# Kernel tuning notes

Hardware: AMD Instinct MI355X
Metric: run time of the kernel (lower is better)

The kernel has to match this reference:

```python
import jax, jax.numpy as jnp
import numpy as np
from functools import partial

L, H, D, T_MAX = 12, 12, 768, 256
HD = D // H
FULL = 302  # 100+100+30+72
LN_EPS = 1e-5


def _ln(x, g, b):
    m = jnp.mean(x, axis=-1, keepdims=True)
    v = jnp.mean((x - m) ** 2, axis=-1, keepdims=True)
    return (x - m) * jax.lax.rsqrt(v + LN_EPS) * g + b


def setup_inputs() -> dict:
    key = jax.random.key(0)
    ks = iter(jax.random.split(key, 40))
    B, T = 64, 256
    w = lambda *s: jax.random.normal(next(ks), s, dtype=jnp.float32) * 0.02
    inp = {
        'idxs': jax.random.randint(next(ks), (B, T, 4), 0, 30, dtype=jnp.int32),
        'lat_emb': w(100, 192), 'lon_emb': w(100, 192),
        'sog_emb': w(30, 192), 'cog_emb': w(72, 192),
        'pos_emb': jnp.zeros((1, T_MAX, D), jnp.float32),
        'ln1_g': jnp.ones((L, D)), 'ln1_b': jnp.zeros((L, D)),
        'ln2_g': jnp.ones((L, D)), 'ln2_b': jnp.zeros((L, D)),
        'Wq': w(L, D, D), 'bq': jnp.zeros((L, D)),
        'Wk': w(L, D, D), 'bk': jnp.zeros((L, D)),
        'Wv': w(L, D, D), 'bv': jnp.zeros((L, D)),
        'Wo': w(L, D, D), 'bo': jnp.zeros((L, D)),
        'W1': w(L, D, 4 * D), 'b1': jnp.zeros((L, 4 * D)),
        'W2': w(L, 4 * D, D), 'b2': jnp.zeros((L, D)),
        'lnf_g': jnp.ones((D,)), 'lnf_b': jnp.zeros((D,)),
        'Whead': w(D, FULL),
    }
    return inp


def _transformer(idxs, lat_emb, lon_emb, sog_emb, cog_emb, pos_emb,
                 ln1_g, ln1_b, ln2_g, ln2_b, Wq, bq, Wk, bk, Wv, bv, Wo, bo,
                 W1, b1, W2, b2, lnf_g, lnf_b, Whead):
    B, T, _ = idxs.shape
    # four-hot embedding: concat of the four attribute embeddings -> [B,T,768]
    h = jnp.concatenate([
        lat_emb[idxs[..., 0]], lon_emb[idxs[..., 1]],
        sog_emb[idxs[..., 2]], cog_emb[idxs[..., 3]],
    ], axis=-1) + pos_emb[:, :T]
    causal = jnp.tril(jnp.ones((T, T), dtype=bool))  # [T,T]
    scale = 1.0 / np.sqrt(HD)

    def block(h, p):
        (g1, b1_, g2, b2_, wq, bq_, wk, bk_, wv, bv_, wo, bo_,
         w1, bf1, w2, bf2) = p
        x = _ln(h, g1, b1_)
        q = (x @ wq + bq_).reshape(B, T, H, HD)
        k = (x @ wk + bk_).reshape(B, T, H, HD)
        v = (x @ wv + bv_).reshape(B, T, H, HD)
        att = jnp.einsum('bqhd,bkhd->bhqk', q, k) * scale
        att = jnp.where(causal, att, -jnp.inf)
        att = jax.nn.softmax(att, axis=-1)
        y = jnp.einsum('bhqk,bkhd->bqhd', att, v).reshape(B, T, D)
        h = h + y @ wo + bo_
        x = _ln(h, g2, b2_)
        h = h + jax.nn.gelu(x @ w1 + bf1, approximate=False) @ w2 + bf2
        return h, None

    stacked = (ln1_g, ln1_b, ln2_g, ln2_b, Wq, bq, Wk, bk, Wv, bv, Wo, bo,
               W1, b1, W2, b2)
    h, _ = jax.lax.scan(block, h, stacked)
    h = _ln(h, lnf_g, lnf_b)
    return h @ Whead  # [B,T,302] logits


def reference(idxs, lat_emb, lon_emb, sog_emb, cog_emb, pos_emb,
              ln1_g, ln1_b, ln2_g, ln2_b, Wq, bq, Wk, bk, Wv, bv, Wo, bo,
              W1, b1, W2, b2, lnf_g, lnf_b, Whead):
    return _transformer(idxs, lat_emb, lon_emb, sog_emb, cog_emb, pos_emb,
                        ln1_g, ln1_b, ln2_g, ln2_b, Wq, bq, Wk, bk, Wv, bv,
                        Wo, bo, W1, b1, W2, b2, lnf_g, lnf_b, Whead)
```

## Files before the change

### kernel.cpp

```cpp
#include <hip/hip_runtime.h>
#include <math.h>


#define LNUM 12
#define HNUM 12
#define DDIM 768
#define HDIM 64
#define TSEQ 256
#define NTOK 16384
#define DFF  3072
#define QKS  1536
#define NOUTC 302
#define NOUTP 384

typedef unsigned short u16;
typedef __attribute__((ext_vector_type(8))) __bf16 bf16x8;
typedef __attribute__((ext_vector_type(8))) unsigned short u16x8;
typedef __attribute__((ext_vector_type(4))) float f32x4;

__device__ __forceinline__ u16 f2bf(float f) {
    union { float f; unsigned u; } v; v.f = f;
    return (u16)((v.u + 0x7fff + ((v.u >> 16) & 1)) >> 16);
}

__device__ __forceinline__ void gl2lds16(const u16* g, u16* l) {
    __builtin_amdgcn_global_load_lds(
        (const __attribute__((address_space(1))) void*)g,
        (__attribute__((address_space(3))) void*)l, 16, 0, 0);
}

__global__ __launch_bounds__(256)
void embed_kernel(const int* __restrict__ idxs, const float* __restrict__ lat,
                  const float* __restrict__ lon, const float* __restrict__ sog,
                  const float* __restrict__ cog, const float* __restrict__ pos,
                  float* __restrict__ h) {
    int i = blockIdx.x * 256 + threadIdx.x;
    int tok = i / DDIM, d = i - tok * DDIM;
    int t = tok & (TSEQ - 1);
    int tab = d / 192, sub = d - tab * 192;
    const float* tp = (tab == 0) ? lat : (tab == 1) ? lon : (tab == 2) ? sog : cog;
    int row = idxs[tok * 4 + tab];
    h[i] = tp[row * 192 + sub] + pos[t * DDIM + d];
}

__global__ __launch_bounds__(256)
void ln_kernel(const float* __restrict__ in, u16* __restrict__ out,
               const float* __restrict__ g, const float* __restrict__ b) {
    const int row = blockIdx.x, t = threadIdx.x;
    const float* x = in + (size_t)row * DDIM;
    float v0 = x[t], v1 = x[t + 256], v2 = x[t + 512];
    float s = v0 + v1 + v2;
    float sq = v0 * v0 + v1 * v1 + v2 * v2;
    #pragma unroll
    for (int m = 32; m; m >>= 1) { s += __shfl_xor(s, m); sq += __shfl_xor(sq, m); }
    __shared__ float red[8];
    const int w = t >> 6;
    if ((t & 63) == 0) { red[w] = s; red[4 + w] = sq; }
    __syncthreads();
    s  = red[0] + red[1] + red[2] + red[3];
    sq = red[4] + red[5] + red[6] + red[7];
    const float mean = s * (1.f / DDIM);
    const float rstd = rsqrtf(sq * (1.f / DDIM) - mean * mean + 1e-5f);
    u16* o = out + (size_t)row * DDIM;
    o[t]       = f2bf((v0 - mean) * rstd * g[t]       + b[t]);
    o[t + 256] = f2bf((v1 - mean) * rstd * g[t + 256] + b[t + 256]);
    o[t + 512] = f2bf((v2 - mean) * rstd * g[t + 512] + b[t + 512]);
}

__global__ __launch_bounds__(256)
void wconv_kernel(const float* __restrict__ in, u16* __restrict__ out,
                  int R, int C, int Cpad) {
    __shared__ float tile[32][33];
    const float* src = in + (size_t)blockIdx.z * R * C;
    u16* dst = out + (size_t)blockIdx.z * (size_t)Cpad * R;
    const int c0 = blockIdx.x * 32, r0 = blockIdx.y * 32;
    const int tx = threadIdx.x & 31, ty = threadIdx.x >> 5;
    #pragma unroll
    for (int i = 0; i < 4; ++i) {
        int r = r0 + ty + i * 8, c = c0 + tx;
        tile[ty + i * 8][tx] = (c < C) ? src[(size_t)r * C + c] : 0.f;
    }
    __syncthreads();
    #pragma unroll
    for (int i = 0; i < 4; ++i) {
        int oc = c0 + ty + i * 8;
        dst[(size_t)oc * R + r0 + tx] = f2bf(tile[tx][ty + i * 8]);
    }
}

template <int MODE>
__global__ __launch_bounds__(256)
void gemm_bt(const u16* __restrict__ A, const u16* __restrict__ Bt,
             const float* __restrict__ bias, const float* __restrict__ bias2,
             const float* __restrict__ bias3, const float* __restrict__ res,
             void* __restrict__ Cout, int M, int N, int K, int ncut) {
    __shared__ u16 As[3][128][32] __attribute__((aligned(16)));
    __shared__ u16 Bs[3][128][32] __attribute__((aligned(16)));
    const int t = threadIdx.x;
    const int w = t >> 6, lane = t & 63;
    const int bm = blockIdx.x * 128, bn = blockIdx.y * 128;
    const int moff = (w >> 1) * 64, noff = (w & 1) * 64;
    const int lrow = t >> 2, lcol = (t & 3) * 8;
    const int fm = lane & 15, fq = lane >> 4;
    const f32x4 zero = {0.f, 0.f, 0.f, 0.f};
    f32x4 acc[4][4];
    #pragma unroll
    for (int a = 0; a < 4; ++a)
        #pragma unroll
        for (int c = 0; c < 4; ++c) acc[a][c] = zero;
    const u16* pA = A + (size_t)(bm + lrow) * K + lcol;
    const u16* pB = Bt + (size_t)(bn + lrow) * K + lcol;
    const size_t rstep = (size_t)64 * K;
    const int wr = w << 4;
    auto stage = [&](int s, int b) {
        const u16* ga = pA + s * 32;
        const u16* gb = pB + s * 32;
        gl2lds16(ga,         &As[b][wr][0]);
        gl2lds16(ga + rstep, &As[b][wr + 64][0]);
        gl2lds16(gb,         &Bs[b][wr][0]);
        gl2lds16(gb + rstep, &Bs[b][wr + 64][0]);
    };
    const int kts = K >> 5;
    stage(0, 0);
    stage(1, 1);
    int bcur = 0, bpre = 2;
    for (int kt = 0; kt < kts; ++kt) {
        if (kt + 2 < kts) stage(kt + 2, bpre);
        const int ahead = kts - 1 - kt;
        if (ahead >= 2)      asm volatile("s_waitcnt vmcnt(8)" ::: "memory");
        else if (ahead == 1) asm volatile("s_waitcnt vmcnt(4)" ::: "memory");
        else                 asm volatile("s_waitcnt vmcnt(0)" ::: "memory");
        __builtin_amdgcn_s_barrier();
        bf16x8 af[4], bfr[4];
        #pragma unroll
        for (int mt = 0; mt < 4; ++mt)
            af[mt] = __builtin_bit_cast(bf16x8, *(const u16x8*)&As[bcur][moff + mt * 16 + fm][fq * 8]);
        #pragma unroll
        for (int nt = 0; nt < 4; ++nt)
            bfr[nt] = __builtin_bit_cast(bf16x8, *(const u16x8*)&Bs[bcur][noff + nt * 16 + fm][fq * 8]);
        asm volatile("s_waitcnt lgkmcnt(0)" ::: "memory");
        __builtin_amdgcn_s_barrier();
        #pragma unroll
        for (int mt = 0; mt < 4; ++mt)
            #pragma unroll
            for (int nt = 0; nt < 4; ++nt)
                acc[mt][nt] = __builtin_amdgcn_mfma_f32_16x16x32_bf16(af[mt], bfr[nt], acc[mt][nt], 0, 0, 0);
        bcur = (bcur == 2) ? 0 : bcur + 1;
        bpre = (bpre == 2) ? 0 : bpre + 1;
    }
    #pragma unroll
    for (int mt = 0; mt < 4; ++mt) {
        #pragma unroll
        for (int nt = 0; nt < 4; ++nt) {
            const int col = bn + noff + nt * 16 + fm;
            float bv = 0.f;
            if (MODE == 5) {
                bv = (col < 768) ? bias[col] : (col < 1536) ? bias2[col - 768] : bias3[col - 1536];
            } else if (MODE != 3) {
                bv = bias[col];
            }
            #pragma unroll
            for (int i = 0; i < 4; ++i) {
                const int row = bm + moff + mt * 16 + fq * 4 + i;
                float v = acc[mt][nt][i] + bv;
                if (MODE == 0) {
                    ((u16*)Cout)[(size_t)row * N + col] = f2bf(v);
                } else if (MODE == 1) {
                    v = 0.5f * v * (1.f + erff(v * 0.70710678118654752f));
                    ((u16*)Cout)[(size_t)row * N + col] = f2bf(v);
                } else if (MODE == 2) {
                    ((float*)Cout)[(size_t)row * N + col] = v + res[(size_t)row * N + col];
                } else if (MODE == 3) {
                    if (col < ncut) ((float*)Cout)[(size_t)row * ncut + col] = v;
                } else {
                    if (col < 1536) {
                        ((u16*)Cout)[(size_t)row * QKS + col] = f2bf(v);
                    } else {
                        const int c = col - 1536;
                        const int bb = row >> 8, tt = row & 255;
                        const int hh = c >> 6, dd = c & 63;
                        u16* vt = (u16*)Cout + (size_t)NTOK * QKS;
                        vt[(((size_t)(bb * HNUM + hh)) * HDIM + dd) * TSEQ + tt] = f2bf(v);
                    }
                }
            }
        }
    }
}

__global__ __launch_bounds__(256)
void attn_kernel(const u16* __restrict__ QK, const u16* __restrict__ Vt,
                 u16* __restrict__ Yb) {
    __shared__ u16 Pt[4][256][16] __attribute__((aligned(16)));
    const int bh = blockIdx.x;
    const int b = bh / HNUM, hh = bh - b * HNUM;
    const int w = threadIdx.x >> 6, lane = threadIdx.x & 63;
    const int fm = lane & 15, fq = lane >> 4;
    const int qt = blockIdx.y * 4 + w;
    const size_t qrow0 = (size_t)b * TSEQ;
    const int col0 = hh * HDIM;
    const u16* qp = QK + (qrow0 + qt * 16 + fm) * QKS + col0 + fq * 8;
    const bf16x8 aq0 = __builtin_bit_cast(bf16x8, *(const u16x8*)qp);
    const bf16x8 aq1 = __builtin_bit_cast(bf16x8, *(const u16x8*)(qp + 32));
    f32x4 s[16];
    #pragma unroll
    for (int kt = 0; kt < 16; ++kt) {
        if (kt <= qt) {
            const u16* kp = QK + (qrow0 + kt * 16 + fm) * QKS + 768 + col0 + fq * 8;
            bf16x8 bk0 = __builtin_bit_cast(bf16x8, *(const u16x8*)kp);
            bf16x8 bk1 = __builtin_bit_cast(bf16x8, *(const u16x8*)(kp + 32));
            f32x4 z = {0.f, 0.f, 0.f, 0.f};
            z = __builtin_amdgcn_mfma_f32_16x16x32_bf16(aq0, bk0, z, 0, 0, 0);
            z = __builtin_amdgcn_mfma_f32_16x16x32_bf16(aq1, bk1, z, 0, 0, 0);
            s[kt] = z;
        }
    }
    float lrow[4];
    #pragma unroll
    for (int i = 0; i < 4; ++i) {
        float mx = -1e30f;
        #pragma unroll
        for (int kt = 0; kt < 16; ++kt) {
            if (kt <= qt) {
                const bool valid = (kt < qt) || (fm <= fq * 4 + i);
                const float v = valid ? s[kt][i] * 0.125f : -1e30f;
                s[kt][i] = v;
                mx = fmaxf(mx, v);
            }
        }
        #pragma unroll
        for (int d = 1; d < 16; d <<= 1) mx = fmaxf(mx, __shfl_xor(mx, d));
        float sum = 0.f;
        #pragma unroll
        for (int kt = 0; kt < 16; ++kt) {
            if (kt <= qt) {
                const float e = __expf(s[kt][i] - mx);
                s[kt][i] = e;
                sum += e;
            }
        }
        #pragma unroll
        for (int d = 1; d < 16; d <<= 1) sum += __shfl_xor(sum, d);
        lrow[i] = sum;
    }
    const int nks = (qt + 2) >> 1;
    #pragma unroll
    for (int kt = 0; kt < 16; ++kt) {
        if (kt < 2 * nks) {
            unsigned lo = 0, hi = 0;
            if (kt <= qt) {
                lo = (unsigned)f2bf(s[kt][0]) | ((unsigned)f2bf(s[kt][1]) << 16);
                hi = (unsigned)f2bf(s[kt][2]) | ((unsigned)f2bf(s[kt][3]) << 16);
            }
            uint2 pk; pk.x = lo; pk.y = hi;
            *(uint2*)&Pt[w][kt * 16 + fm][fq * 4] = pk;
        }
    }
    __syncthreads();
    f32x4 o[4];
    #pragma unroll
    for (int dt = 0; dt < 4; ++dt) o[dt] = (f32x4){0.f, 0.f, 0.f, 0.f};
    #pragma unroll
    for (int ks = 0; ks < 8; ++ks) {
        if (ks < nks) {
            u16x8 praw;
            #pragma unroll
            for (int j = 0; j < 8; ++j) praw[j] = Pt[w][ks * 32 + fq * 8 + j][fm];
            const bf16x8 pa = __builtin_bit_cast(bf16x8, praw);
            #pragma unroll
            for (int dt = 0; dt < 4; ++dt) {
                const u16* vp = Vt + ((size_t)bh * HDIM + dt * 16 + fm) * TSEQ + ks * 32 + fq * 8;
                const bf16x8 bv = __builtin_bit_cast(bf16x8, *(const u16x8*)vp);
                o[dt] = __builtin_amdgcn_mfma_f32_16x16x32_bf16(pa, bv, o[dt], 0, 0, 0);
            }
        }
    }
    #pragma unroll
    for (int i = 0; i < 4; ++i) {
        const float inv = 1.f / lrow[i];
        #pragma unroll
        for (int dt = 0; dt < 4; ++dt)
            Yb[(qrow0 + qt * 16 + fq * 4 + i) * DDIM + col0 + dt * 16 + fm] = f2bf(o[dt][i] * inv);
    }
}

extern "C" void kernel_launch(void* const* d_in, const int* in_sizes, int n_in,
                              void* d_out, int out_size, void* d_ws, size_t ws_size,
                              hipStream_t stream) {
    (void)in_sizes; (void)n_in; (void)out_size; (void)ws_size;
    const int*   idxs  = (const int*)d_in[0];
    const float* lat   = (const float*)d_in[1];
    const float* lon   = (const float*)d_in[2];
    const float* sog   = (const float*)d_in[3];
    const float* cog   = (const float*)d_in[4];
    const float* pos   = (const float*)d_in[5];
    const float* ln1_g = (const float*)d_in[6];
    const float* ln1_b = (const float*)d_in[7];
    const float* ln2_g = (const float*)d_in[8];
    const float* ln2_b = (const float*)d_in[9];
    const float* Wq = (const float*)d_in[10];
    const float* bq = (const float*)d_in[11];
    const float* Wk = (const float*)d_in[12];
    const float* bk = (const float*)d_in[13];
    const float* Wv = (const float*)d_in[14];
    const float* bv = (const float*)d_in[15];
    const float* Wo = (const float*)d_in[16];
    const float* bo = (const float*)d_in[17];
    const float* W1 = (const float*)d_in[18];
    const float* b1 = (const float*)d_in[19];
    const float* W2 = (const float*)d_in[20];
    const float* b2 = (const float*)d_in[21];
    const float* lnf_g = (const float*)d_in[22];
    const float* lnf_b = (const float*)d_in[23];
    const float* Whead = (const float*)d_in[24];

    char* base = (char*)d_ws;
    size_t off = 0;
    auto carve = [&](size_t bytes) { void* r = base + off; off += (bytes + 255) & ~(size_t)255; return r; };
    float* h  = (float*)carve((size_t)NTOK * DDIM * 4);
    u16* xb = (u16*)carve((size_t)NTOK * DDIM * 2);
    u16* qk = (u16*)carve((size_t)NTOK * QKS * 2);
    u16* vt = (u16*)carve((size_t)NTOK * DDIM * 2);
    u16* yb = (u16*)carve((size_t)NTOK * DDIM * 2);
    u16* ub = qk;
    u16* WtQKV = (u16*)carve((size_t)3 * DDIM * DDIM * 2);
    u16* WtO = (u16*)carve((size_t)DDIM * DDIM * 2);
    u16* Wt1 = (u16*)carve((size_t)DDIM * DFF * 2);
    u16* Wt2 = (u16*)carve((size_t)DFF * DDIM * 2);
    u16* WtH = (u16*)carve((size_t)NOUTP * DDIM * 2);

    embed_kernel<<<NTOK * DDIM / 256, 256, 0, stream>>>(idxs, lat, lon, sog, cog, pos, h);

    const dim3 g768(128, 6), g3072(128, 24), gqkv(128, 18), ghead(128, 3);
    const dim3 tq(24, 24, 1), t1(96, 24, 1), t2(24, 96, 1);
    const size_t wsq = (size_t)DDIM * DDIM, wsf = (size_t)DDIM * DFF;
    for (int l = 0; l < LNUM; ++l) {
        wconv_kernel<<<tq, 256, 0, stream>>>(Wq + l * wsq, WtQKV, DDIM, DDIM, DDIM);
        wconv_kernel<<<tq, 256, 0, stream>>>(Wk + l * wsq, WtQKV + wsq, DDIM, DDIM, DDIM);
        wconv_kernel<<<tq, 256, 0, stream>>>(Wv + l * wsq, WtQKV + 2 * wsq, DDIM, DDIM, DDIM);
        wconv_kernel<<<tq, 256, 0, stream>>>(Wo + l * wsq, WtO, DDIM, DDIM, DDIM);
        wconv_kernel<<<t1, 256, 0, stream>>>(W1 + l * wsf, Wt1, DDIM, DFF, DFF);
        wconv_kernel<<<t2, 256, 0, stream>>>(W2 + l * wsf, Wt2, DFF, DDIM, DDIM);

        ln_kernel<<<NTOK, 256, 0, stream>>>(h, xb, ln1_g + l * DDIM, ln1_b + l * DDIM);
        gemm_bt<5><<<gqkv, 256, 0, stream>>>(xb, WtQKV, bq + l * DDIM, bk + l * DDIM,
                                             bv + l * DDIM, nullptr, qk,
                                             NTOK, 3 * DDIM, DDIM, 0);
        attn_kernel<<<dim3(768, 4), 256, 0, stream>>>(qk, vt, yb);
        gemm_bt<2><<<g768, 256, 0, stream>>>(yb, WtO, bo + l * DDIM, nullptr, nullptr, h, h,
                                             NTOK, DDIM, DDIM, 0);
        ln_kernel<<<NTOK, 256, 0, stream>>>(h, xb, ln2_g + l * DDIM, ln2_b + l * DDIM);
        gemm_bt<1><<<g3072, 256, 0, stream>>>(xb, Wt1, b1 + l * DFF, nullptr, nullptr, nullptr, ub,
                                              NTOK, DFF, DDIM, 0);
        gemm_bt<2><<<g768, 256, 0, stream>>>(ub, Wt2, b2 + l * DDIM, nullptr, nullptr, h, h,
                                             NTOK, DDIM, DFF, 0);
    }
    ln_kernel<<<NTOK, 256, 0, stream>>>(h, xb, lnf_g, lnf_b);
    wconv_kernel<<<dim3(NOUTP / 32, DDIM / 32, 1), 256, 0, stream>>>(Whead, WtH, DDIM, NOUTC, NOUTP);
    gemm_bt<3><<<ghead, 256, 0, stream>>>(xb, WtH, nullptr, nullptr, nullptr, nullptr, d_out,
                                          NTOK, NOUTP, DDIM, NOUTC);
}
```

Measured before the change: 6.656 ms.

## Replace 128x128 GEMMs with 256x256-tile 8-wave kernel using direct global-to-LDS loads

Adds a gemm256 kernel with 256x256 output tiles, 512 threads (8 waves), K-step 64, and double-buffered LDS filled through direct global-to-LDS copies with an XOR-swizzled layout. It interleaves MFMA quadrants with staged loads, uses explicit vmcnt waits, s_setprio, and an XCD-aware block remap. The aim is more data reuse per tile and better overlap of loads with compute for the QKV, output-projection and MLP GEMMs. The cost is heavy register use (128 accumulator floats per thread), only 64x3 blocks for the 768-wide GEMMs, and reliance on the gl2lds16 helper and hand-tuned barriers being correct.

```diff
diff --git a/kernel.cpp b/kernel.cpp
--- a/kernel.cpp
+++ b/kernel.cpp
@@ -85,6 +85,135 @@
     for (int i = 0; i < 4; ++i) {
         int oc = c0 + ty + i * 8;
         dst[(size_t)oc * R + r0 + tx] = f2bf(tile[tx][ty + i * 8]);
+    }
+}
+
+
+#define LDA8(MQ) \
+  _Pragma("unroll") for (int mt = 0; mt < 4; ++mt) { \
+    a[mt][0] = __builtin_bit_cast(bf16x8, *(const u16x8*)(A0p + (MQ)*8192 + mt*1024)); \
+    a[mt][1] = __builtin_bit_cast(bf16x8, *(const u16x8*)(A1p + (MQ)*8192 + mt*1024)); }
+
+#define LDB4(NQ, BR) \
+  _Pragma("unroll") for (int nt = 0; nt < 2; ++nt) { \
+    BR[nt][0] = __builtin_bit_cast(bf16x8, *(const u16x8*)(B0p + (NQ)*8192 + nt*1024)); \
+    BR[nt][1] = __builtin_bit_cast(bf16x8, *(const u16x8*)(B1p + (NQ)*8192 + nt*1024)); }
+
+#define MMA16(MQ, NQ, BR) \
+  __builtin_amdgcn_s_barrier(); \
+  asm volatile("s_waitcnt lgkmcnt(0)" ::: "memory"); \
+  __builtin_amdgcn_s_setprio(1); \
+  _Pragma("unroll") for (int mt = 0; mt < 4; ++mt) \
+  _Pragma("unroll") for (int nt = 0; nt < 2; ++nt) { \
+    acc[(MQ)*4+mt][(NQ)*2+nt] = __builtin_amdgcn_mfma_f32_16x16x32_bf16(a[mt][0], BR[nt][0], acc[(MQ)*4+mt][(NQ)*2+nt], 0, 0, 0); \
+    acc[(MQ)*4+mt][(NQ)*2+nt] = __builtin_amdgcn_mfma_f32_16x16x32_bf16(a[mt][1], BR[nt][1], acc[(MQ)*4+mt][(NQ)*2+nt], 0, 0, 0); } \
+  __builtin_amdgcn_s_setprio(0);
+
+#define STGA(NXT, H, KT) { \
+  const u16* s_ = gA + (size_t)((H) * 128) * K + (size_t)(KT) * 64; \
+  u16* d_ = &Sh[NXT][H][0][0] + w * 512; \
+  gl2lds16(s_, d_); gl2lds16(s_ + (size_t)64 * K, d_ + 4096); }
+
+#define STGB(NXT, H, KT) { \
+  const u16* s_ = gB + (size_t)((H) * 128) * K + (size_t)(KT) * 64; \
+  u16* d_ = &Sh[NXT][2 + (H)][0][0] + w * 512; \
+  gl2lds16(s_, d_); gl2lds16(s_ + (size_t)64 * K, d_ + 4096); }
+
+#define VM4 asm volatile("s_waitcnt vmcnt(4)" ::: "memory");
+#define VM2 asm volatile("s_waitcnt vmcnt(2)" ::: "memory");
+#define VM0 asm volatile("s_waitcnt vmcnt(0)" ::: "memory");
+#define VMN
+
+#define KTILE(CUR, KT, STG, VA, VB, VC) { \
+  const u16* A0p = aQ0 + (CUR) * 32768; const u16* A1p = aQ1 + (CUR) * 32768; \
+  const u16* B0p = bQ0 + (CUR) * 32768; const u16* B1p = bQ1 + (CUR) * 32768; \
+   LDA8(0) LDB4(0, b0) if (STG) STGA(1 - (CUR), 0, (KT) + 1) \
+         MMA16(0, 0, b0) VA __builtin_amdgcn_s_barrier(); \
+   LDB4(1, b1) if (STG) STGB(1 - (CUR), 0, (KT) + 1) \
+         MMA16(0, 1, b1) VB __builtin_amdgcn_s_barrier(); \
+   LDA8(1) if (STG) STGB(1 - (CUR), 1, (KT) + 1) \
+         MMA16(1, 1, b1) __builtin_amdgcn_s_barrier(); \
+   if (STG) STGA(1 - (CUR), 1, (KT) + 1) \
+         MMA16(1, 0, b0) VC __builtin_amdgcn_s_barrier(); \
+}
+
+template <int MODE>
+__global__ __launch_bounds__(512, 2)
+void gemm256(const u16* __restrict__ A, const u16* __restrict__ Bt,
+             const float* __restrict__ bias, const float* __restrict__ bias2,
+             const float* __restrict__ bias3, const float* __restrict__ res,
+             void* __restrict__ Cout, int M, int N, int K) {
+    (void)M;
+    __shared__ u16 Sh[2][4][128][64] __attribute__((aligned(16)));
+    const int t = threadIdx.x;
+    const int w = t >> 6, l = t & 63;
+    const int wm = w >> 2, wn = w & 3;
+    const int fm = l & 15, fq = l >> 4;
+    const int nwg = (int)(gridDim.x * gridDim.y);
+    int lin = (int)(blockIdx.y * gridDim.x + blockIdx.x);
+    const int cpx = nwg >> 3;
+    lin = (lin & 7) * cpx + (lin >> 3);
+    const int bm = (lin & 63) * 256, bn = (lin >> 6) * 256;
+    const int srow = (w << 3) + (l >> 3);
+    const int schunk = (l & 7) ^ ((l >> 3) & 7);
+    const u16* gA = A + (size_t)(bm + srow) * K + schunk * 8;
+    const u16* gB = Bt + (size_t)(bn + srow) * K + schunk * 8;
+    const int aoff0 = fm * 64 + ((fq ^ (fm & 7)) << 3);
+    const int aoff1 = aoff0 ^ 32;
+    const u16* aQ0 = &Sh[0][0][0][0] + wm * 4096 + aoff0;
+    const u16* aQ1 = &Sh[0][0][0][0] + wm * 4096 + aoff1;
+    const u16* bQ0 = &Sh[0][2][0][0] + wn * 2048 + aoff0;
+    const u16* bQ1 = &Sh[0][2][0][0] + wn * 2048 + aoff1;
+    f32x4 acc[8][4];
+    #pragma unroll
+    for (int i = 0; i < 8; ++i)
+        #pragma unroll
+        for (int j = 0; j < 4; ++j) acc[i][j] = (f32x4){0.f, 0.f, 0.f, 0.f};
+    bf16x8 a[4][2], b0[2][2], b1[2][2];
+    STGA(0, 0, 0) STGB(0, 0, 0) STGB(0, 1, 0) STGA(0, 1, 0)
+    asm volatile("s_waitcnt vmcnt(4)" ::: "memory");
+    __builtin_amdgcn_s_barrier();
+    const int nkt = K >> 6;
+    for (int kt = 0; kt < nkt - 2; kt += 2) {
+        KTILE(0, kt,     true, VM4, VM4, VM4)
+        KTILE(1, kt + 1, true, VM4, VM4, VM4)
+    }
+    KTILE(0, nkt - 2, true,  VM4, VM4, VM4)
+    KTILE(1, nkt - 1, false, VM2, VM0, VMN)
+    #pragma unroll
+    for (int m8 = 0; m8 < 8; ++m8) {
+        const int row0 = bm + (m8 >> 2) * 128 + wm * 64 + (m8 & 3) * 16 + fq * 4;
+        #pragma unroll
+        for (int n4 = 0; n4 < 4; ++n4) {
+            const int col = bn + (n4 >> 1) * 128 + wn * 32 + (n4 & 1) * 16 + fm;
+            float bv;
+            if (MODE == 5) {
+                bv = (col < 768) ? bias[col] : (col < 1536) ? bias2[col - 768] : bias3[col - 1536];
+            } else {
+                bv = bias[col];
+            }
+            #pragma unroll
+            for (int i = 0; i < 4; ++i) {
+                const int row = row0 + i;
+                float v = acc[m8][n4][i] + bv;
+                if (MODE == 1) {
+                    v = 0.5f * v * (1.f + erff(v * 0.70710678118654752f));
+                    ((u16*)Cout)[(size_t)row * N + col] = f2bf(v);
+                } else if (MODE == 2) {
+                    ((float*)Cout)[(size_t)row * N + col] = v + res[(size_t)row * N + col];
+                } else {
+                    if (col < 1536) {
+                        ((u16*)Cout)[(size_t)row * QKS + col] = f2bf(v);
+                    } else {
+                        const int c = col - 1536;
+                        const int bb = row >> 8, tt = row & 255;
+                        const int hh = c >> 6, dd = c & 63;
+                        u16* vt = (u16*)Cout + (size_t)NTOK * QKS;
+                        vt[(((size_t)(bb * HNUM + hh)) * HDIM + dd) * TSEQ + tt] = f2bf(v);
+                    }
+                }
+            }
+        }
     }
 }
 
@@ -331,7 +460,7 @@
 
     embed_kernel<<<NTOK * DDIM / 256, 256, 0, stream>>>(idxs, lat, lon, sog, cog, pos, h);
 
-    const dim3 g768(128, 6), g3072(128, 24), gqkv(128, 18), ghead(128, 3);
+    const dim3 G768(64, 3), G3072(64, 12), GQKV(64, 9), ghead(128, 3);
     const dim3 tq(24, 24, 1), t1(96, 24, 1), t2(24, 96, 1);
     const size_t wsq = (size_t)DDIM * DDIM, wsf = (size_t)DDIM * DFF;
     for (int l = 0; l < LNUM; ++l) {
@@ -343,17 +472,17 @@
         wconv_kernel<<<t2, 256, 0, stream>>>(W2 + l * wsf, Wt2, DFF, DDIM, DDIM);
 
         ln_kernel<<<NTOK, 256, 0, stream>>>(h, xb, ln1_g + l * DDIM, ln1_b + l * DDIM);
-        gemm_bt<5><<<gqkv, 256, 0, stream>>>(xb, WtQKV, bq + l * DDIM, bk + l * DDIM,
+        gemm256<5><<<GQKV, 512, 0, stream>>>(xb, WtQKV, bq + l * DDIM, bk + l * DDIM,
                                              bv + l * DDIM, nullptr, qk,
-                                             NTOK, 3 * DDIM, DDIM, 0);
+                                             NTOK, 3 * DDIM, DDIM);
         attn_kernel<<<dim3(768, 4), 256, 0, stream>>>(qk, vt, yb);
-        gemm_bt<2><<<g768, 256, 0, stream>>>(yb, WtO, bo + l * DDIM, nullptr, nullptr, h, h,
-                                             NTOK, DDIM, DDIM, 0);
+        gemm256<2><<<G768, 512, 0, stream>>>(yb, WtO, bo + l * DDIM, nullptr, nullptr, h, h,
+                                             NTOK, DDIM, DDIM);
         ln_kernel<<<NTOK, 256, 0, stream>>>(h, xb, ln2_g + l * DDIM, ln2_b + l * DDIM);
-        gemm_bt<1><<<g3072, 256, 0, stream>>>(xb, Wt1, b1 + l * DFF, nullptr, nullptr, nullptr, ub,
-                                              NTOK, DFF, DDIM, 0);
-        gemm_bt<2><<<g768, 256, 0, stream>>>(ub, Wt2, b2 + l * DDIM, nullptr, nullptr, h, h,
-                                             NTOK, DDIM, DFF, 0);
+        gemm256<1><<<G3072, 512, 0, stream>>>(xb, Wt1, b1 + l * DFF, nullptr, nullptr, nullptr, ub,
+                                              NTOK, DFF, DDIM);
+        gemm256<2><<<G768, 512, 0, stream>>>(ub, Wt2, b2 + l * DDIM, nullptr, nullptr, h, h,
+                                             NTOK, DDIM, DFF);
     }
     ln_kernel<<<NTOK, 256, 0, stream>>>(h, xb, lnf_g, lnf_b);
     wconv_kernel<<<dim3(NOUTP / 32, DDIM / 32, 1), 256, 0, stream>>>(Whead, WtH, DDIM, NOUTC, NOUTP);
```

Result: slower. 6.789 ms (+2.0%).
